# Kernel tuning notes

Measured on AMD Instinct MI355X. Metric: run time of the kernel, lower is better.

Reference implementation:

```python
import jax, jax.numpy as jnp
import numpy as np

B, T, A, H, E = 512, 64, 32, 512, 32


def sinusoidal_pos_encoding(t, dim):
    # t: (B, T) float positions -> (B, T, dim)
    half = dim // 2
    freqs = jnp.exp(-jnp.log(10000.0) * jnp.arange(half, dtype=jnp.float32) / half)
    ang = t[..., None] * freqs  # (B, T, half)
    return jnp.concatenate([jnp.sin(ang), jnp.cos(ang)], axis=-1)


def cat_linear(x, W, b, cat_ids):
    # x: (B, T, Din); W: (E, Din, Dout); b: (E, Dout); cat_ids: (B,)
    Wg = W[cat_ids]            # (B, Din, Dout) gathered per-sample weights
    bg = b[cat_ids][:, None]   # (B, 1, Dout)
    return jnp.einsum('btd,bdh->bth', x, Wg) + bg


def swish(x):
    return x * jax.nn.sigmoid(x)


def setup_inputs() -> dict:
    key = jax.random.key(0)
    ks = jax.random.split(key, 10)
    s = lambda fan_in: 1.0 / np.sqrt(fan_in)
    return {
        'actions': jax.random.normal(ks[0], (B, T, A), dtype=jnp.float32),
        'timesteps': jax.random.uniform(ks[1], (B,), dtype=jnp.float32),
        'cat_ids': jax.random.randint(ks[2], (B,), 0, E),
        'W1': jax.random.normal(ks[3], (E, A, H), dtype=jnp.float32) * s(A),
        'b1': jnp.zeros((E, H), dtype=jnp.float32),
        'W2': jax.random.normal(ks[4], (E, 2 * H, H), dtype=jnp.float32) * s(2 * H),
        'b2': jnp.zeros((E, H), dtype=jnp.float32),
        'W3': jax.random.normal(ks[5], (E, H, H), dtype=jnp.float32) * s(H),
        'b3': jnp.zeros((E, H), dtype=jnp.float32),
    }


def reference(actions, timesteps, cat_ids, W1, b1, W2, b2, W3, b3):
    b, t, _ = actions.shape
    timesteps_bt = jnp.broadcast_to(timesteps[:, None], (b, t))
    a_emb = cat_linear(actions, W1, b1, cat_ids)              # (B, T, H)
    tau_emb = sinusoidal_pos_encoding(timesteps_bt, H).astype(a_emb.dtype)
    x = jnp.concatenate([a_emb, tau_emb], axis=-1)            # (B, T, 2H)
    x = swish(cat_linear(x, W2, b2, cat_ids))                 # (B, T, H)
    x = cat_linear(x, W3, b3, cat_ids)                        # (B, T, H)
    return x
```

## Files before the change

kernel.cpp:

```cpp
#include <hip/hip_runtime.h>
#include <hip/hip_bf16.h>

#define B_ 512
#define T_ 64
#define A_ 32
#define H_ 512
#define E_ 32
#define MAX_TASKS 160

typedef unsigned short u16;
typedef unsigned int u32;
typedef __attribute__((ext_vector_type(8))) short short8;
typedef __attribute__((ext_vector_type(4))) float floatx4;

static __device__ __forceinline__ u16 f2bf(float f) {
    u32 u = __builtin_bit_cast(u32, f);
    u += 0x7fffu + ((u >> 16) & 1u);
    return (u16)(u >> 16);
}

static __device__ __forceinline__ void gl2lds16(const u16* g, u16* l) {
    __builtin_amdgcn_global_load_lds(
        (const __attribute__((address_space(1))) void*)g,
        (__attribute__((address_space(3))) void*)l, 16, 0, 0);
}

__global__ void group_kernel(const int* __restrict__ cat_ids,
                             int* __restrict__ sample_list,
                             int4* __restrict__ tasks) {
    __shared__ int cnt[E_], off[E_], cur[E_], toff[E_];
    __shared__ int total;
    int tid = threadIdx.x;
    if (tid < E_) { cnt[tid] = 0; cur[tid] = 0; }
    __syncthreads();
    int e = cat_ids[tid];
    atomicAdd(&cnt[e], 1);
    __syncthreads();
    if (tid == 0) {
        int run = 0, trun = 0;
        for (int i = 0; i < E_; i++) {
            off[i] = run;  run += cnt[i];
            toff[i] = trun; trun += (cnt[i] + 3) >> 2;
        }
        total = trun;
    }
    __syncthreads();
    if (tid < E_) {
        int c = cnt[tid], o = off[tid], to = toff[tid];
        for (int j = 0; j < c; j += 4) {
            int ns = c - j; if (ns > 4) ns = 4;
            tasks[to++] = make_int4(tid, o + j, ns, 0);
        }
    }
    for (int i = total + tid; i < MAX_TASKS; i += 512)
        tasks[i] = make_int4(0, 0, 0, 0);
    int p = atomicAdd(&cur[e], 1);
    sample_list[off[e] + p] = tid;
}

__global__ __launch_bounds__(256) void embed_kernel(
        const float* __restrict__ actions, const float* __restrict__ timesteps,
        const int* __restrict__ cat_ids, const float* __restrict__ W1,
        const float* __restrict__ b1, u16* __restrict__ a_emb,
        u16* __restrict__ tau_emb) {
    int b = blockIdx.x;
    int tid = threadIdx.x;
    int e = cat_ids[b];
    float tval = timesteps[b];

    {
        float freq = expf(-9.210340371976184f * (float)tid * (1.0f / 256.0f));
        float ang = tval * freq;
        tau_emb[b * H_ + tid]       = f2bf(sinf(ang));
        tau_emb[b * H_ + 256 + tid] = f2bf(cosf(ang));
    }

    __shared__ float act[T_ * A_];
    const float* asrc = actions + (size_t)b * T_ * A_;
    for (int i = tid; i < T_ * A_; i += 256) act[i] = asrc[i];
    __syncthreads();

    const float* w1 = W1 + (size_t)e * A_ * H_;
    int n0 = tid, n1 = tid + 256;
    float wA[A_], wB[A_];
#pragma unroll
    for (int k = 0; k < A_; k++) {
        wA[k] = w1[k * H_ + n0];
        wB[k] = w1[k * H_ + n1];
    }
    float bA = b1[e * H_ + n0], bB = b1[e * H_ + n1];
    u16* orow = a_emb + (size_t)b * T_ * H_;
    for (int tt = 0; tt < T_; tt++) {
        float accA = bA, accB = bB;
#pragma unroll
        for (int k = 0; k < A_; k++) {
            float a = act[tt * A_ + k];
            accA = fmaf(a, wA[k], accA);
            accB = fmaf(a, wB[k], accB);
        }
        orow[tt * H_ + n0] = f2bf(accA);
        orow[tt * H_ + n1] = f2bf(accB);
    }
}

__global__ __launch_bounds__(256) void convert_transpose(
        const float* __restrict__ W, u16* __restrict__ Wt, int K) {
    int n = blockIdx.y * 256 + threadIdx.x;
    int k0 = blockIdx.x * 32;
    int e = blockIdx.z;
    const float* src = W + ((size_t)e * K + k0) * H_ + n;
    short8 out[4];
#pragma unroll
    for (int j = 0; j < 32; j++)
        out[j >> 3][j & 7] = (short)f2bf(src[(size_t)j * H_]);
    u16* dst = Wt + ((size_t)e * H_ + n) * K + k0;
#pragma unroll
    for (int c = 0; c < 4; c++) *(short8*)(dst + c * 8) = out[c];
}

template <int DIN, bool HAS_TAU, bool DO_SWISH, bool OUT_BF16>
__global__ __launch_bounds__(512, 4) void moe_gemm(
        const u16* __restrict__ xsrc, const u16* __restrict__ tau,
        const u16* __restrict__ Wt, const float* __restrict__ bias,
        const int* __restrict__ sample_list, const int4* __restrict__ tasks,
        void* __restrict__ outp) {
    int4 task = tasks[blockIdx.y];
    int ns = task.z;
    if (ns == 0) return;
    int e = task.x;
    int sl[4];
#pragma unroll
    for (int j = 0; j < 4; j++)
        sl[j] = sample_list[task.y + ((j < ns) ? j : (ns - 1))];
    int n0 = blockIdx.x * 128;

    int tid = threadIdx.x;
    int lane = tid & 63, wv = tid >> 6;
    int wr = wv >> 1, wc = wv & 1;
    int quad = lane >> 4, c15 = lane & 15;
    int r8 = lane >> 3, cg = lane & 7;

    __shared__ __align__(16) u16 xs[256 * 64];
    __shared__ __align__(16) u16 wt[128 * 64];

    floatx4 acc[4][4];
    floatx4 zero4 = {0.f, 0.f, 0.f, 0.f};
#pragma unroll
    for (int i = 0; i < 4; i++)
#pragma unroll
        for (int j = 0; j < 4; j++) acc[i][j] = zero4;

    const u16* wbase = Wt + (size_t)(e * H_ + n0) * DIN;
    int kc_sw = (cg ^ r8) * 8;

    for (int k0 = 0; k0 < DIN; k0 += 64) {
        bool use_tau = HAS_TAU && (k0 >= 512);
#pragma unroll
        for (int j = 0; j < 4; j++) {
            int rg = 8 * wv + 64 * j;
            int t = 8 * wv + r8;
            int s = sl[j];
            const u16* g = use_tau
                ? (tau + (size_t)s * H_ + (k0 - 512) + kc_sw)
                : (xsrc + ((size_t)s * T_ + t) * H_ + k0 + kc_sw);
            gl2lds16(g, &xs[rg * 64]);
        }
#pragma unroll
        for (int i = 0; i < 2; i++) {
            int ng = 8 * wv + 64 * i;
            int nrow = ng + r8;
            const u16* g = wbase + (size_t)nrow * DIN + k0 + kc_sw;
            gl2lds16(g, &wt[ng * 64]);
        }
        __syncthreads();

#pragma unroll
        for (int kk = 0; kk < 2; kk++) {
            int c = kk * 4 + quad;
            short8 af[4], bfr[4];
#pragma unroll
            for (int i = 0; i < 4; i++) {
                int row = wr * 64 + i * 16 + c15;
                af[i] = *(const short8*)&xs[row * 64 + ((c ^ (row & 7)) * 8)];
                int nr = wc * 64 + i * 16 + c15;
                bfr[i] = *(const short8*)&wt[nr * 64 + ((c ^ (nr & 7)) * 8)];
            }
#pragma unroll
            for (int mt = 0; mt < 4; mt++)
#pragma unroll
                for (int nt = 0; nt < 4; nt++)
                    acc[mt][nt] = __builtin_amdgcn_mfma_f32_16x16x32_bf16(
                            af[mt], bfr[nt], acc[mt][nt], 0, 0, 0);
        }
        __syncthreads();
    }

    if (wr >= ns) return;
    int s = sl[wr];
    const float* bp = bias + (size_t)e * H_;
#pragma unroll
    for (int mt = 0; mt < 4; mt++) {
        int tb = mt * 16 + quad * 4;
#pragma unroll
        for (int nt = 0; nt < 4; nt++) {
            int col = n0 + wc * 64 + nt * 16 + c15;
            float bv = bp[col];
#pragma unroll
            for (int r = 0; r < 4; r++) {
                float v = acc[mt][nt][r] + bv;
                if (DO_SWISH) v = v / (1.0f + expf(-v));
                size_t oidx = ((size_t)s * T_ + tb + r) * H_ + col;
                if (OUT_BF16) ((u16*)outp)[oidx] = f2bf(v);
                else          ((float*)outp)[oidx] = v;
            }
        }
    }
}

extern "C" void kernel_launch(void* const* d_in, const int* in_sizes, int n_in,
                              void* d_out, int out_size, void* d_ws, size_t ws_size,
                              hipStream_t stream) {
    const float* actions   = (const float*)d_in[0];
    const float* timesteps = (const float*)d_in[1];
    const int*   cat_ids   = (const int*)d_in[2];
    const float* W1 = (const float*)d_in[3];
    const float* b1 = (const float*)d_in[4];
    const float* W2 = (const float*)d_in[5];
    const float* b2 = (const float*)d_in[6];
    const float* W3 = (const float*)d_in[7];
    const float* b3 = (const float*)d_in[8];

    char* ws = (char*)d_ws;
    u16* a_emb = (u16*)ws;
    u16* y     = (u16*)(ws + (size_t)32 * 1024 * 1024);
    u16* tau   = (u16*)(ws + (size_t)64 * 1024 * 1024);
    int* sample_list = (int*)(ws + (size_t)64 * 1024 * 1024 + 512 * 1024);
    int4* tasks = (int4*)(ws + (size_t)64 * 1024 * 1024 + 512 * 1024 + 4096);
    u16* Wt2 = (u16*)d_out;
    u16* Wt3 = a_emb;

    hipLaunchKernelGGL(group_kernel, dim3(1), dim3(512), 0, stream,
                       cat_ids, sample_list, tasks);
    hipLaunchKernelGGL(embed_kernel, dim3(512), dim3(256), 0, stream,
                       actions, timesteps, cat_ids, W1, b1, a_emb, tau);
    hipLaunchKernelGGL(convert_transpose, dim3(2 * H_ / 32, 2, E_), dim3(256),
                       0, stream, W2, Wt2, 2 * H_);
    hipLaunchKernelGGL((moe_gemm<2 * H_, true, true, true>), dim3(4, MAX_TASKS),
                       dim3(512), 0, stream,
                       a_emb, tau, Wt2, b2, sample_list, tasks, (void*)y);
    hipLaunchKernelGGL(convert_transpose, dim3(H_ / 32, 2, E_), dim3(256),
                       0, stream, W3, Wt3, H_);
    hipLaunchKernelGGL((moe_gemm<H_, false, false, false>), dim3(4, MAX_TASKS),
                       dim3(512), 0, stream,
                       y, (const u16*)nullptr, Wt3, b3, sample_list, tasks, d_out);
}
```

Before: 323.0 us.

## Shrink MoE GEMM tiles to 2 samples and schedule items per XCD

Tasks now group at most 2 samples per expert instead of 4, so each GEMM block handles a 128x128 tile with 256 threads instead of 256x128 with 512. The group kernel builds a flattened item list that assigns an expert's tiles to blocks in a round-robin pattern over 8 slots, so blocks sharing an expert's weights likely land on the same XCD and its L2. If any slot overflows its capacity it falls back to a linear order. The aim is less padding waste for experts with odd sample counts, more blocks for parallelism, and better weight cache reuse, at the cost of reloading each weight tile for twice as many tasks.

```diff
diff --git a/kernel.cpp b/kernel.cpp
--- a/kernel.cpp
+++ b/kernel.cpp
@@ -6,7 +6,9 @@
 #define A_ 32
 #define H_ 512
 #define E_ 32
-#define MAX_TASKS 160
+#define MAX_TASKS 272
+#define CAP_ 168
+#define GRID_ (8 * CAP_)
 
 typedef unsigned short u16;
 typedef unsigned int u32;
@@ -27,9 +29,10 @@
 
 __global__ void group_kernel(const int* __restrict__ cat_ids,
                              int* __restrict__ sample_list,
-                             int4* __restrict__ tasks) {
-    __shared__ int cnt[E_], off[E_], cur[E_], toff[E_];
-    __shared__ int total;
+                             int4* __restrict__ tasks,
+                             int* __restrict__ itemlist) {
+    __shared__ int cnt[E_], off[E_], cur[E_], toff[E_], jc[8];
+    __shared__ int total, fb;
     int tid = threadIdx.x;
     if (tid < E_) { cnt[tid] = 0; cur[tid] = 0; }
     __syncthreads();
@@ -40,20 +43,46 @@
         int run = 0, trun = 0;
         for (int i = 0; i < E_; i++) {
             off[i] = run;  run += cnt[i];
-            toff[i] = trun; trun += (cnt[i] + 3) >> 2;
+            toff[i] = trun; trun += (cnt[i] + 1) >> 1;
         }
         total = trun;
     }
     __syncthreads();
     if (tid < E_) {
         int c = cnt[tid], o = off[tid], to = toff[tid];
-        for (int j = 0; j < c; j += 4) {
-            int ns = c - j; if (ns > 4) ns = 4;
-            tasks[to++] = make_int4(tid, o + j, ns, 0);
-        }
-    }
-    for (int i = total + tid; i < MAX_TASKS; i += 512)
-        tasks[i] = make_int4(0, 0, 0, 0);
+        for (int j = 0; j < c; j += 2)
+            tasks[to++] = make_int4(tid, o + j, (c - j >= 2) ? 2 : 1, 0);
+    }
+    if (tid < 8) {
+        int J = 0;
+        for (int cc = 0; cc < 4; cc++) J += 4 * ((cnt[tid + 8 * cc] + 1) >> 1);
+        jc[tid] = J;
+    }
+    __syncthreads();
+    if (tid == 0) {
+        int f = 0;
+        for (int x = 0; x < 8; x++) if (jc[x] > CAP_) f = 1;
+        fb = f;
+    }
+    __syncthreads();
+    if (!fb) {
+        if (tid < 8) {
+            int j = 0;
+            for (int cc = 0; cc < 4; cc++) {
+                int ee = tid + 8 * cc;
+                int nt = (cnt[ee] + 1) >> 1, t0 = toff[ee];
+                for (int t = t0; t < t0 + nt; t++)
+                    for (int nb = 0; nb < 4; nb++) {
+                        itemlist[tid + 8 * j] = (t << 2) | nb;
+                        j++;
+                    }
+            }
+            for (; j < CAP_; j++) itemlist[tid + 8 * j] = -1;
+        }
+    } else {
+        for (int f = tid; f < GRID_; f += 512)
+            itemlist[f] = (f < 4 * total) ? f : -1;
+    }
     int p = atomicAdd(&cur[e], 1);
     sample_list[off[e] + p] = tid;
 }
@@ -119,20 +148,20 @@
 }
 
 template <int DIN, bool HAS_TAU, bool DO_SWISH, bool OUT_BF16>
-__global__ __launch_bounds__(512, 4) void moe_gemm(
+__global__ __launch_bounds__(256, 4) void moe_gemm(
         const u16* __restrict__ xsrc, const u16* __restrict__ tau,
         const u16* __restrict__ Wt, const float* __restrict__ bias,
         const int* __restrict__ sample_list, const int4* __restrict__ tasks,
-        void* __restrict__ outp) {
-    int4 task = tasks[blockIdx.y];
+        const int* __restrict__ itemlist, void* __restrict__ outp) {
+    int item = itemlist[blockIdx.x];
+    if (item < 0) return;
+    int4 task = tasks[item >> 2];
+    int nb = item & 3;
     int ns = task.z;
-    if (ns == 0) return;
     int e = task.x;
-    int sl[4];
-#pragma unroll
-    for (int j = 0; j < 4; j++)
-        sl[j] = sample_list[task.y + ((j < ns) ? j : (ns - 1))];
-    int n0 = blockIdx.x * 128;
+    int s0 = sample_list[task.y];
+    int s1 = (ns > 1) ? sample_list[task.y + 1] : s0;
+    int n0 = nb * 128;
 
     int tid = threadIdx.x;
     int lane = tid & 63, wv = tid >> 6;
@@ -140,7 +169,7 @@
     int quad = lane >> 4, c15 = lane & 15;
     int r8 = lane >> 3, cg = lane & 7;
 
-    __shared__ __align__(16) u16 xs[256 * 64];
+    __shared__ __align__(16) u16 xs[128 * 64];
     __shared__ __align__(16) u16 wt[128 * 64];
 
     floatx4 acc[4][4];
@@ -156,21 +185,21 @@
     for (int k0 = 0; k0 < DIN; k0 += 64) {
         bool use_tau = HAS_TAU && (k0 >= 512);
 #pragma unroll
-        for (int j = 0; j < 4; j++) {
-            int rg = 8 * wv + 64 * j;
-            int t = 8 * wv + r8;
-            int s = sl[j];
+        for (int h = 0; h < 4; h++) {
+            int rbase = h * 32 + wv * 8;
+            int row = rbase + r8;
+            int s = (rbase < 64) ? s0 : s1;
+            int t = row & 63;
             const u16* g = use_tau
                 ? (tau + (size_t)s * H_ + (k0 - 512) + kc_sw)
                 : (xsrc + ((size_t)s * T_ + t) * H_ + k0 + kc_sw);
-            gl2lds16(g, &xs[rg * 64]);
-        }
-#pragma unroll
-        for (int i = 0; i < 2; i++) {
-            int ng = 8 * wv + 64 * i;
-            int nrow = ng + r8;
-            const u16* g = wbase + (size_t)nrow * DIN + k0 + kc_sw;
-            gl2lds16(g, &wt[ng * 64]);
+            gl2lds16(g, &xs[rbase * 64]);
+        }
+#pragma unroll
+        for (int h = 0; h < 4; h++) {
+            int nbase = h * 32 + wv * 8;
+            int nrow = nbase + r8;
+            gl2lds16(wbase + (size_t)nrow * DIN + k0 + kc_sw, &wt[nbase * 64]);
         }
         __syncthreads();
 
@@ -196,7 +225,7 @@
     }
 
     if (wr >= ns) return;
-    int s = sl[wr];
+    int s = (wr == 0) ? s0 : s1;
     const float* bp = bias + (size_t)e * H_;
 #pragma unroll
     for (int mt = 0; mt < 4; mt++) {
@@ -234,23 +263,26 @@
     u16* a_emb = (u16*)ws;
     u16* y     = (u16*)(ws + (size_t)32 * 1024 * 1024);
     u16* tau   = (u16*)(ws + (size_t)64 * 1024 * 1024);
-    int* sample_list = (int*)(ws + (size_t)64 * 1024 * 1024 + 512 * 1024);
-    int4* tasks = (int4*)(ws + (size_t)64 * 1024 * 1024 + 512 * 1024 + 4096);
+    char* meta = ws + (size_t)64 * 1024 * 1024 + 512 * 1024;
+    int*  sample_list = (int*)meta;
+    int4* tasks       = (int4*)(meta + 8192);
+    int*  itemlist    = (int*)(meta + 16384);
     u16* Wt2 = (u16*)d_out;
     u16* Wt3 = a_emb;
 
     hipLaunchKernelGGL(group_kernel, dim3(1), dim3(512), 0, stream,
-                       cat_ids, sample_list, tasks);
+                       cat_ids, sample_list, tasks, itemlist);
     hipLaunchKernelGGL(embed_kernel, dim3(512), dim3(256), 0, stream,
                        actions, timesteps, cat_ids, W1, b1, a_emb, tau);
     hipLaunchKernelGGL(convert_transpose, dim3(2 * H_ / 32, 2, E_), dim3(256),
                        0, stream, W2, Wt2, 2 * H_);
-    hipLaunchKernelGGL((moe_gemm<2 * H_, true, true, true>), dim3(4, MAX_TASKS),
-                       dim3(512), 0, stream,
-                       a_emb, tau, Wt2, b2, sample_list, tasks, (void*)y);
+    hipLaunchKernelGGL((moe_gemm<2 * H_, true, true, true>), dim3(GRID_),
+                       dim3(256), 0, stream,
+                       a_emb, tau, Wt2, b2, sample_list, tasks, itemlist, (void*)y);
     hipLaunchKernelGGL(convert_transpose, dim3(H_ / 32, 2, E_), dim3(256),
                        0, stream, W3, Wt3, H_);
-    hipLaunchKernelGGL((moe_gemm<H_, false, false, false>), dim3(4, MAX_TASKS),
-                       dim3(512), 0, stream,
-                       y, (const u16*)nullptr, Wt3, b3, sample_list, tasks, d_out);
-}
+    hipLaunchKernelGGL((moe_gemm<H_, false, false, false>), dim3(GRID_),
+                       dim3(256), 0, stream,
+                       y, (const u16*)nullptr, Wt3, b3, sample_list, tasks,
+                       itemlist, d_out);
+}
```

After: 315.8 us. -2.2%, faster.
